# Performance work log

Hardware: AMD Instinct MI355X
Metric: run time of the kernel (lower is better)

Reference implementation:

```python
import jax, jax.numpy as jnp
import numpy as np

N_LAYERS, B, H, D = 24, 16, 32, 64
E = H * D            # 2048
TS_H = 32            # token_shift_hidden_dim
N_BRANCH = 5         # key, receptance, decay, value, bonus
GN_EPS = 1e-3        # keras GroupNormalization default epsilon


def setup_inputs() -> dict:
    key = jax.random.key(0)
    ks = jax.random.split(key, 20)
    s = 0.02
    return {
        "inputs": jax.random.normal(ks[0], (B, E), jnp.float32),
        "state": jax.random.normal(ks[1], (N_LAYERS, 1, B, E), jnp.float32),
        "state_matrix": jax.random.normal(ks[2], (N_LAYERS, B, H, D, D), jnp.float32),
        # stacked branch params, order: key, receptance, decay, value, bonus
        "mus": jax.random.normal(ks[3], (N_BRANCH, E), jnp.float32) * s,
        "lambdas": jax.random.normal(ks[4], (N_BRANCH, E), jnp.float32) * s,
        "Aw": jax.random.normal(ks[5], (N_BRANCH, E, TS_H), jnp.float32) * s,
        "Ab": jnp.zeros((N_BRANCH, TS_H), jnp.float32),
        "Bw": jax.random.normal(ks[6], (N_BRANCH, TS_H, E), jnp.float32) * s,
        "Bb": jnp.zeros((N_BRANCH, E), jnp.float32),
        "MW": jax.random.normal(ks[7], (N_BRANCH, H, D, D), jnp.float32) * s,
        "Mb": jnp.zeros((N_BRANCH, H, D), jnp.float32),
        "gate_mu": jax.random.normal(ks[8], (E,), jnp.float32) * s,
        "gate_W": jax.random.normal(ks[9], (E, E), jnp.float32) * s,
        "gate_b": jnp.zeros((E,), jnp.float32),
        "gn_gamma": jnp.ones((E,), jnp.float32),
        "gn_beta": jnp.zeros((E,), jnp.float32),
        "out_W": jax.random.normal(ks[10], (E, E), jnp.float32) * s,
        "out_b": jnp.zeros((E,), jnp.float32),
        "layer_id": 12,
    }


def reference(inputs, state, state_matrix, mus, lambdas, Aw, Ab, Bw, Bb, MW, Mb,
              gate_mu, gate_W, gate_b, gn_gamma, gn_beta, out_W, out_b, layer_id):
    x = inputs                       # [B, E]
    last_x = state[layer_id, 0]      # [B, E]
    diff = x - last_x

    # ddlerp token shift for all 5 branches at once:
    # lora(x + diff*mu) = lambda + tanh(. @ A) @ B ; out = x + lora * diff
    lora_in = x[None] + diff[None] * mus[:, None]                      # [5, B, E]
    hdn = jnp.tanh(jnp.einsum('sbe,seh->sbh', lora_in, Aw) + Ab[:, None])
    lora = jnp.einsum('sbh,she->sbe', hdn, Bw) + Bb[:, None] + lambdas[:, None]
    ts = (lora * diff[None] + x[None]).reshape(N_BRANCH, B, H, D)      # [5, B, H, D]

    # per-head dense for each branch
    proj = jnp.einsum('sbhd,shde->sbhe', ts, MW) + Mb[:, None]         # [5, B, H, D]
    k, r, w_raw, v, u = proj[0], proj[1], proj[2], proj[3], proj[4]

    g = (x * gate_mu + last_x * (1.0 - gate_mu)) @ gate_W + gate_b     # [B, E]

    kv = k[..., :, None] * v[..., None, :]                             # [B, H, D, D]
    w = jnp.exp(-jnp.exp(w_raw))[..., None]                            # [B, H, D, 1]
    S = state_matrix[layer_id]                                         # [B, H, D, D]
    wkv = kv * u[..., None] + S
    new_S = w * S + kv
    rwkv = jnp.einsum('bhij,bhj->bhi', wkv, r)                         # [B, H, D]

    # group norm: num_heads groups over channel axis
    mean = rwkv.mean(-1, keepdims=True)
    var = rwkv.var(-1, keepdims=True)
    normed = ((rwkv - mean) / jnp.sqrt(var + GN_EPS)).reshape(B, E)
    normed = normed * gn_gamma + gn_beta

    time_mixed = (normed * jax.nn.silu(g)) @ out_W + out_b             # [B, E]

    new_state = state.at[layer_id, 0].set(inputs)
    new_state_matrix = state_matrix.at[layer_id].set(new_S)
    return time_mixed, new_state, new_state_matrix
```

## Files before the change

### kernel.cpp

```cpp
#include <hip/hip_runtime.h>
#include <math.h>

#define NL 24
#define BB 16
#define HH 32
#define DD 64
#define EE 2048
#define TSH 32
#define NB 5
#define BE (BB*EE)
#define STATE_N (NL*BB*EE)
#define GN_EPS 1e-3f

#define NCH 11776
#define C1 2700
#define C2 2500
#define C3 2100
#define C4 2400
#define C5 2076

typedef float nt4 __attribute__((ext_vector_type(4)));

__device__ __forceinline__ void sm_chunk(int c, int lid, const nt4* __restrict__ sm4,
                                         nt4* __restrict__ out4, int tid) {
    int l = c >> 9, rr = c & 511;
    int ls = l + (l >= lid);
    const nt4* src = sm4 + (long)(ls * 512 + rr) * 1024;
    nt4*       dst = out4 + (long)(ls * 512 + rr) * 1024;
    #pragma unroll
    for (int p = 0; p < 4; ++p) {
        nt4 v = __builtin_nontemporal_load(&src[p * 256 + tid]);
        __builtin_nontemporal_store(v, &dst[p * 256 + tid]);
    }
}

__global__ __launch_bounds__(256) void k1_hdn(
    const float* __restrict__ inputs, const float* __restrict__ state,
    const float* __restrict__ mus, const float* __restrict__ Aw,
    const float* __restrict__ Ab, float* __restrict__ hdn,
    const nt4* __restrict__ state4, const float4* __restrict__ inputs4,
    nt4* __restrict__ out_state4, float* __restrict__ out_tm,
    float* __restrict__ g, const float* __restrict__ out_b,
    const float* __restrict__ gate_b, const float* __restrict__ gate_mu,
    float* __restrict__ gx,
    const nt4* __restrict__ sm4, nt4* __restrict__ out_sm4,
    const int* __restrict__ lid_p)
{
    int blk = blockIdx.x, tid = threadIdx.x;
    int lid = *lid_p;
    if (blk >= 1232) {
        sm_chunk(blk - 1232, lid, sm4, out_sm4, tid);
        return;
    }
    if (blk >= 848) {
        int idx = (blk - 848) * 256 + tid;
        if (idx < BE) out_tm[idx] = out_b[idx & (EE - 1)];
        else if (idx < 2 * BE) g[idx - BE] = gate_b[(idx - BE) & (EE - 1)];
        else {
            int r = idx - 2 * BE;
            float xv = inputs[r];
            float lxv = state[lid * BE + r];
            float gm = gate_mu[r & (EE - 1)];
            gx[r] = xv * gm + lxv * (1.f - gm);
        }
        return;
    }
    if (blk >= 80) {
        int i = (blk - 80) * 256 + tid;
        int lo = lid * (BE / 4);
        if (i >= lo && i < lo + BE / 4) {
            float4 v = inputs4[i - lo];
            nt4 w = { v.x, v.y, v.z, v.w };
            __builtin_nontemporal_store(w, &out_state4[i]);
        } else {
            nt4 v = __builtin_nontemporal_load(&state4[i]);
            __builtin_nontemporal_store(v, &out_state4[i]);
        }
        return;
    }
    int s = blk / BB, b = blk % BB;
    __shared__ float li[EE];
    const float* x  = inputs + b * EE;
    const float* lx = state + lid * BE + b * EE;
    const float* mu = mus + s * EE;
    for (int e = tid; e < EE; e += 256) {
        float xv = x[e];
        li[e] = xv + (xv - lx[e]) * mu[e];
    }
    __syncthreads();
    int h = tid & 31, part = tid >> 5;
    const float* A = Aw + s * EE * TSH;
    float acc = 0.f;
    int e0 = part * 256;
    #pragma unroll 8
    for (int e = e0; e < e0 + 256; ++e) acc += li[e] * A[e * TSH + h];
    __shared__ float red[32][9];
    red[h][part] = acc;
    __syncthreads();
    if (tid < 32) {
        float sum = Ab[s * TSH + tid];
        #pragma unroll
        for (int p = 0; p < 8; ++p) sum += red[tid][p];
        hdn[(s * BB + b) * TSH + tid] = tanhf(sum);
    }
}

__global__ __launch_bounds__(256) void k2_ts(
    const float* __restrict__ inputs, const float* __restrict__ state,
    const float* __restrict__ lambdas, const float* __restrict__ Bw,
    const float* __restrict__ Bb, const float* __restrict__ hdn,
    float* __restrict__ ts,
    const nt4* __restrict__ sm4, nt4* __restrict__ out_sm4,
    const int* __restrict__ lid_p)
{
    int blk = blockIdx.x, tid = threadIdx.x;
    int lid = *lid_p;
    if (blk >= 640) {
        sm_chunk(C1 + blk - 640, lid, sm4, out_sm4, tid);
        return;
    }
    int idx = blk * 256 + tid;
    int s = idx / BE, r = idx % BE;
    int b = r / EE, e = r % EE;
    const float* hp = hdn + (s * BB + b) * TSH;
    const float* Bp = Bw + s * TSH * EE + e;
    float acc = Bb[s * EE + e] + lambdas[s * EE + e];
    #pragma unroll
    for (int h = 0; h < TSH; ++h) acc += hp[h] * Bp[h * EE];
    float xv = inputs[r];
    float lxv = state[lid * BE + r];
    ts[idx] = acc * (xv - lxv) + xv;
}

template <bool SILU>
__device__ __forceinline__ void mm_block(
    int t, const float* __restrict__ Arows, const float* __restrict__ Grows,
    const float* __restrict__ W, float* __restrict__ out, int tid)
{
    int et = t & 7, kc = t >> 3;
    int e = et * 256 + tid;
    int k0 = kc * 64;
    __shared__ float As[BB][64];
    for (int i = tid; i < BB * 64; i += 256) {
        int b = i >> 6, kk = i & 63;
        float av = Arows[b * EE + k0 + kk];
        if constexpr (SILU) {
            float gv = Grows[b * EE + k0 + kk];
            av *= gv / (1.f + expf(-gv));
        }
        As[b][kk] = av;
    }
    __syncthreads();
    float acc[BB];
    #pragma unroll
    for (int b = 0; b < BB; ++b) acc[b] = 0.f;
    #pragma unroll 8
    for (int kk = 0; kk < 64; ++kk) {
        float wv = W[(k0 + kk) * EE + e];
        #pragma unroll
        for (int b = 0; b < BB; ++b) acc[b] += As[b][kk] * wv;
    }
    #pragma unroll
    for (int b = 0; b < BB; ++b) atomicAdd(&out[b * EE + e], acc[b]);
}

__global__ __launch_bounds__(256) void k3_proj(
    const float* __restrict__ ts, const float* __restrict__ MW,
    const float* __restrict__ Mb, float* __restrict__ proj,
    const float* __restrict__ gx, const float* __restrict__ gate_W,
    float* __restrict__ g,
    const nt4* __restrict__ sm4, nt4* __restrict__ out_sm4,
    const int* __restrict__ lid_p)
{
    int bi = blockIdx.x, tid = threadIdx.x;
    if (bi >= 896) {
        int lid = *lid_p;
        sm_chunk(C1 + C2 + bi - 896, lid, sm4, out_sm4, tid);
        return;
    }
    if (bi >= 640) {
        mm_block<false>(bi - 640, gx, nullptr, gate_W, g, tid);
        return;
    }
    int s = bi / (BB * 8);
    int r = bi % (BB * 8);
    int b = r / 8, hg = r % 8;
    int q = tid >> 6, e = tid & 63;
    int h = hg * 4 + q;
    __shared__ float tl[4][DD];
    tl[q][e] = ts[((s * BB + b) * HH + h) * DD + e];
    __syncthreads();
    const float* M = MW + (s * HH + h) * DD * DD;
    float acc = Mb[(s * HH + h) * DD + e];
    #pragma unroll 8
    for (int d = 0; d < DD; ++d) acc += tl[q][d] * M[d * DD + e];
    proj[((s * BB + b) * HH + h) * DD + e] = acc;
}

__global__ __launch_bounds__(256) void k4_rwkv(
    const float4* __restrict__ sm4, float4* __restrict__ out_sm4,
    const float* __restrict__ proj,
    const float* __restrict__ gn_gamma, const float* __restrict__ gn_beta,
    float* __restrict__ a_out, const int* __restrict__ lid_p)
{
    int blk = blockIdx.x, tid = threadIdx.x;
    int lid = *lid_p;
    if (blk >= 512) {
        sm_chunk(C1 + C2 + C3 + blk - 512, lid,
                 (const nt4*)sm4, (nt4*)out_sm4, tid);
        return;
    }
    int b = blk / HH, h = blk % HH;
    long base4 = (long)(lid * BB * HH + blk) * (DD * DD / 4);
    int j = tid & 63, q = tid >> 6;
    const float* P = proj + (b * HH + h) * DD + j;
    float kv   = P[0 * BE];
    float rv   = P[1 * BE];
    float wraw = P[2 * BE];
    float vv   = P[3 * BE];
    float uv   = P[4 * BE];
    float wv = expf(-expf(wraw));
    float vr = vv * rv;
    #pragma unroll
    for (int o = 32; o; o >>= 1) vr += __shfl_xor(vr, o);
    __shared__ float rw[DD];
    const float* S = (const float*)(sm4 + base4);
    float* NS = (float*)(out_sm4 + base4);
    for (int ii = 0; ii < 16; ii += 4) {
        int i0 = q * 16 + ii;
        float sv[4], kk[4], ww[4], uu[4], pp[4];
        #pragma unroll
        for (int t = 0; t < 4; ++t) {
            sv[t] = S[(i0 + t) * DD + j];
            kk[t] = __shfl(kv, i0 + t);
            ww[t] = __shfl(wv, i0 + t);
            uu[t] = __shfl(uv, i0 + t);
        }
        #pragma unroll
        for (int t = 0; t < 4; ++t) {
            NS[(i0 + t) * DD + j] = ww[t] * sv[t] + kk[t] * vv;
            pp[t] = sv[t] * rv;
        }
        #pragma unroll
        for (int o = 32; o; o >>= 1) {
            #pragma unroll
            for (int t = 0; t < 4; ++t) pp[t] += __shfl_xor(pp[t], o);
        }
        if (j == 0) {
            #pragma unroll
            for (int t = 0; t < 4; ++t) rw[i0 + t] = kk[t] * uu[t] * vr + pp[t];
        }
    }
    __syncthreads();
    if (tid < DD) {
        float xv = rw[tid];
        float m = xv;
        #pragma unroll
        for (int o = 32; o; o >>= 1) m += __shfl_xor(m, o);
        m *= (1.f / 64.f);
        float d = xv - m;
        float var = d * d;
        #pragma unroll
        for (int o = 32; o; o >>= 1) var += __shfl_xor(var, o);
        var *= (1.f / 64.f);
        float normed = d * rsqrtf(var + GN_EPS);
        int e = h * DD + tid;
        a_out[b * EE + e] = normed * gn_gamma[e] + gn_beta[e];
    }
}

__global__ __launch_bounds__(256) void k5_out(
    const float* __restrict__ a, const float* __restrict__ g,
    const float* __restrict__ out_W, float* __restrict__ out_tm,
    const nt4* __restrict__ sm4, nt4* __restrict__ out_sm4,
    const int* __restrict__ lid_p)
{
    int blk = blockIdx.x, tid = threadIdx.x;
    if (blk < 256) { mm_block<true>(blk, a, g, out_W, out_tm, tid); return; }
    int lid = *lid_p;
    sm_chunk(C1 + C2 + C3 + C4 + blk - 256, lid, sm4, out_sm4, tid);
}

extern "C" void kernel_launch(void* const* d_in, const int* in_sizes, int n_in,
                              void* d_out, int out_size, void* d_ws, size_t ws_size,
                              hipStream_t stream) {
    const float* inputs   = (const float*)d_in[0];
    const float* state    = (const float*)d_in[1];
    const float* sm       = (const float*)d_in[2];
    const float* mus      = (const float*)d_in[3];
    const float* lambdas  = (const float*)d_in[4];
    const float* Aw       = (const float*)d_in[5];
    const float* Ab       = (const float*)d_in[6];
    const float* Bw       = (const float*)d_in[7];
    const float* Bb       = (const float*)d_in[8];
    const float* MW       = (const float*)d_in[9];
    const float* Mb       = (const float*)d_in[10];
    const float* gate_mu  = (const float*)d_in[11];
    const float* gate_W   = (const float*)d_in[12];
    const float* gate_b   = (const float*)d_in[13];
    const float* gn_gamma = (const float*)d_in[14];
    const float* gn_beta  = (const float*)d_in[15];
    const float* out_W    = (const float*)d_in[16];
    const float* out_b    = (const float*)d_in[17];
    const int*   lid      = (const int*)d_in[18];

    float* out_tm    = (float*)d_out;
    float* out_state = out_tm + BE;
    float* out_sm    = out_state + STATE_N;

    float* ws   = (float*)d_ws;
    float* ts   = ws;
    float* proj = ts + NB * BE;
    float* hdn  = proj + NB * BE;
    float* gx   = hdn + NB * BB * TSH;
    float* g    = gx + BE;
    float* a    = g + BE;

    k1_hdn<<<1232 + C1, 256, 0, stream>>>(inputs, state, mus, Aw, Ab, hdn,
        (const nt4*)state, (const float4*)inputs, (nt4*)out_state,
        out_tm, g, out_b, gate_b, gate_mu, gx,
        (const nt4*)sm, (nt4*)out_sm, lid);
    k2_ts<<<640 + C2, 256, 0, stream>>>(inputs, state, lambdas, Bw, Bb, hdn,
        ts, (const nt4*)sm, (nt4*)out_sm, lid);
    k3_proj<<<896 + C3, 256, 0, stream>>>(ts, MW, Mb, proj, gx, gate_W, g,
        (const nt4*)sm, (nt4*)out_sm, lid);
    k4_rwkv<<<512 + C4, 256, 0, stream>>>((const float4*)sm, (float4*)out_sm,
        proj, gn_gamma, gn_beta, a, lid);
    k5_out<<<256 + C5, 256, 0, stream>>>(a, g, out_W, out_tm,
        (const nt4*)sm, (nt4*)out_sm, lid);
}
```

Measured before the change: 436.9 us.

## Fuse token-shift LoRA and per-head projection into one kernel

```diff
diff --git a/kernel.cpp b/kernel.cpp
--- a/kernel.cpp
+++ b/kernel.cpp
@@ -13,11 +13,10 @@
 #define GN_EPS 1e-3f
 
 #define NCH 11776
-#define C1 2700
-#define C2 2500
-#define C3 2100
-#define C4 2400
-#define C5 2076
+#define C1 3300
+#define C2 3200
+#define C3 3200
+#define C4 2076
 
 typedef float nt4 __attribute__((ext_vector_type(4)));
 
@@ -105,33 +104,6 @@
     }
 }
 
-__global__ __launch_bounds__(256) void k2_ts(
-    const float* __restrict__ inputs, const float* __restrict__ state,
-    const float* __restrict__ lambdas, const float* __restrict__ Bw,
-    const float* __restrict__ Bb, const float* __restrict__ hdn,
-    float* __restrict__ ts,
-    const nt4* __restrict__ sm4, nt4* __restrict__ out_sm4,
-    const int* __restrict__ lid_p)
-{
-    int blk = blockIdx.x, tid = threadIdx.x;
-    int lid = *lid_p;
-    if (blk >= 640) {
-        sm_chunk(C1 + blk - 640, lid, sm4, out_sm4, tid);
-        return;
-    }
-    int idx = blk * 256 + tid;
-    int s = idx / BE, r = idx % BE;
-    int b = r / EE, e = r % EE;
-    const float* hp = hdn + (s * BB + b) * TSH;
-    const float* Bp = Bw + s * TSH * EE + e;
-    float acc = Bb[s * EE + e] + lambdas[s * EE + e];
-    #pragma unroll
-    for (int h = 0; h < TSH; ++h) acc += hp[h] * Bp[h * EE];
-    float xv = inputs[r];
-    float lxv = state[lid * BE + r];
-    ts[idx] = acc * (xv - lxv) + xv;
-}
-
 template <bool SILU>
 __device__ __forceinline__ void mm_block(
     int t, const float* __restrict__ Arows, const float* __restrict__ Grows,
@@ -164,40 +136,58 @@
     for (int b = 0; b < BB; ++b) atomicAdd(&out[b * EE + e], acc[b]);
 }
 
-__global__ __launch_bounds__(256) void k3_proj(
-    const float* __restrict__ ts, const float* __restrict__ MW,
-    const float* __restrict__ Mb, float* __restrict__ proj,
+__global__ __launch_bounds__(256) void k2_tsproj(
+    const float* __restrict__ inputs, const float* __restrict__ state,
+    const float* __restrict__ lambdas, const float* __restrict__ Bw,
+    const float* __restrict__ Bb, const float* __restrict__ hdn,
+    const float* __restrict__ MW, const float* __restrict__ Mb,
+    float* __restrict__ proj,
     const float* __restrict__ gx, const float* __restrict__ gate_W,
     float* __restrict__ g,
     const nt4* __restrict__ sm4, nt4* __restrict__ out_sm4,
     const int* __restrict__ lid_p)
 {
-    int bi = blockIdx.x, tid = threadIdx.x;
-    if (bi >= 896) {
+    int blk = blockIdx.x, tid = threadIdx.x;
+    if (blk >= 896) {
         int lid = *lid_p;
-        sm_chunk(C1 + C2 + bi - 896, lid, sm4, out_sm4, tid);
-        return;
-    }
-    if (bi >= 640) {
-        mm_block<false>(bi - 640, gx, nullptr, gate_W, g, tid);
-        return;
-    }
-    int s = bi / (BB * 8);
-    int r = bi % (BB * 8);
+        sm_chunk(C1 + blk - 896, lid, sm4, out_sm4, tid);
+        return;
+    }
+    if (blk >= 640) {
+        mm_block<false>(blk - 640, gx, nullptr, gate_W, g, tid);
+        return;
+    }
+    int lid = *lid_p;
+    int s = blk / (BB * 8);
+    int r = blk % (BB * 8);
     int b = r / 8, hg = r % 8;
-    int q = tid >> 6, e = tid & 63;
+    int e = hg * 256 + tid;
+    __shared__ float hl[TSH];
+    __shared__ float tsl[256];
+    if (tid < TSH) hl[tid] = hdn[(s * BB + b) * TSH + tid];
+    __syncthreads();
+    {
+        int ge = b * EE + e;
+        const float* Bp = Bw + s * TSH * EE + e;
+        float acc = Bb[s * EE + e] + lambdas[s * EE + e];
+        #pragma unroll
+        for (int h = 0; h < TSH; ++h) acc += hl[h] * Bp[h * EE];
+        float xv = inputs[ge];
+        float lxv = state[lid * BE + ge];
+        tsl[tid] = acc * (xv - lxv) + xv;
+    }
+    __syncthreads();
+    int q = tid >> 6, e2 = tid & 63;
     int h = hg * 4 + q;
-    __shared__ float tl[4][DD];
-    tl[q][e] = ts[((s * BB + b) * HH + h) * DD + e];
-    __syncthreads();
     const float* M = MW + (s * HH + h) * DD * DD;
-    float acc = Mb[(s * HH + h) * DD + e];
+    const float* t = tsl + q * DD;
+    float acc = Mb[(s * HH + h) * DD + e2];
     #pragma unroll 8
-    for (int d = 0; d < DD; ++d) acc += tl[q][d] * M[d * DD + e];
-    proj[((s * BB + b) * HH + h) * DD + e] = acc;
-}
-
-__global__ __launch_bounds__(256) void k4_rwkv(
+    for (int d = 0; d < DD; ++d) acc += t[d] * M[d * DD + e2];
+    proj[((s * BB + b) * HH + h) * DD + e2] = acc;
+}
+
+__global__ __launch_bounds__(256) void k3_rwkv(
     const float4* __restrict__ sm4, float4* __restrict__ out_sm4,
     const float* __restrict__ proj,
     const float* __restrict__ gn_gamma, const float* __restrict__ gn_beta,
@@ -206,7 +196,7 @@
     int blk = blockIdx.x, tid = threadIdx.x;
     int lid = *lid_p;
     if (blk >= 512) {
-        sm_chunk(C1 + C2 + C3 + blk - 512, lid,
+        sm_chunk(C1 + C2 + blk - 512, lid,
                  (const nt4*)sm4, (nt4*)out_sm4, tid);
         return;
     }
@@ -269,7 +259,7 @@
     }
 }
 
-__global__ __launch_bounds__(256) void k5_out(
+__global__ __launch_bounds__(256) void k4_out(
     const float* __restrict__ a, const float* __restrict__ g,
     const float* __restrict__ out_W, float* __restrict__ out_tm,
     const nt4* __restrict__ sm4, nt4* __restrict__ out_sm4,
@@ -278,7 +268,7 @@
     int blk = blockIdx.x, tid = threadIdx.x;
     if (blk < 256) { mm_block<true>(blk, a, g, out_W, out_tm, tid); return; }
     int lid = *lid_p;
-    sm_chunk(C1 + C2 + C3 + C4 + blk - 256, lid, sm4, out_sm4, tid);
+    sm_chunk(C1 + C2 + C3 + blk - 256, lid, sm4, out_sm4, tid);
 }
 
 extern "C" void kernel_launch(void* const* d_in, const int* in_sizes, int n_in,
@@ -309,8 +299,7 @@
     float* out_sm    = out_state + STATE_N;
 
     float* ws   = (float*)d_ws;
-    float* ts   = ws;
-    float* proj = ts + NB * BE;
+    float* proj = ws;
     float* hdn  = proj + NB * BE;
     float* gx   = hdn + NB * BB * TSH;
     float* g    = gx + BE;
@@ -320,12 +309,11 @@
         (const nt4*)state, (const float4*)inputs, (nt4*)out_state,
         out_tm, g, out_b, gate_b, gate_mu, gx,
         (const nt4*)sm, (nt4*)out_sm, lid);
-    k2_ts<<<640 + C2, 256, 0, stream>>>(inputs, state, lambdas, Bw, Bb, hdn,
-        ts, (const nt4*)sm, (nt4*)out_sm, lid);
-    k3_proj<<<896 + C3, 256, 0, stream>>>(ts, MW, Mb, proj, gx, gate_W, g,
+    k2_tsproj<<<896 + C2, 256, 0, stream>>>(inputs, state, lambdas, Bw, Bb, hdn,
+        MW, Mb, proj, gx, gate_W, g,
         (const nt4*)sm, (nt4*)out_sm, lid);
-    k4_rwkv<<<512 + C4, 256, 0, stream>>>((const float4*)sm, (float4*)out_sm,
+    k3_rwkv<<<512 + C3, 256, 0, stream>>>((const float4*)sm, (float4*)out_sm,
         proj, gn_gamma, gn_beta, a, lid);
-    k5_out<<<256 + C5, 256, 0, stream>>>(a, g, out_W, out_tm,
+    k4_out<<<256 + C4, 256, 0, stream>>>(a, g, out_W, out_tm,
         (const nt4*)sm, (nt4*)out_sm, lid);
 }
```

New measurement: 429.1 us. No clear change (-1.8%).
